# Kernel tuning notes

Measured on AMD Instinct MI355X. Metric: run time of the kernel, lower is better.

## Reference

```python
import jax, jax.numpy as jnp
import numpy as np

B, P, D, E, A, V, T = 128, 49, 512, 512, 512, 10000, 50


def _lstm_cell(x, h, c, w_ih, w_hh, b_ih, b_hh):
    # torch.nn.LSTMCell gate order: i, f, g, o
    g = x @ w_ih.T + b_ih + h @ w_hh.T + b_hh
    i, f, gg, o = jnp.split(g, 4, axis=1)
    c_new = jax.nn.sigmoid(f) * c + jax.nn.sigmoid(i) * jnp.tanh(gg)
    h_new = jax.nn.sigmoid(o) * jnp.tanh(c_new)
    return h_new, c_new


def _forward(spatial_feature, global_image, emb, w_ih1, w_hh1, b_ih1, b_hh1,
             s_wx, s_bx, s_wh, s_bh, w_ih2, w_hh2, b_ih2, b_hh2,
             aff_s_w, aff_s_b, aff_h_w, aff_h_b, ws_w, ws_b, wg_w, wg_b,
             wv_w, wv_b, wh_w, wh_b, wp_w, wp_b, fc_w, fc_b, encoded_captions):
    Bz, Tz = encoded_captions.shape
    embs = jnp.take(emb, encoded_captions, axis=0)                 # (B, T, E)
    gi = jnp.broadcast_to(global_image[:, None, :], (Bz, Tz, global_image.shape[-1]))
    x_word = jnp.concatenate([embs, gi], axis=-1)[:, :-1]          # (B, T-1, 2E) = [w_t; v^g]
    visual_att = spatial_feature @ wv_w.T + wv_b                   # (B, P, A); loop-invariant, hoisted

    def step(carry, x_t):
        h1, m1, h2, m2 = carry
        # ---- LSTM-1 on [h_last^2; w_t; v^g] ----
        x1 = jnp.concatenate([h2, x_t], axis=1)                    # (B, D + 2E)
        h1n, m1n = _lstm_cell(x1, h1, m1, w_ih1, w_hh1, b_ih1, b_hh1)
        # visual sentinel (dropout = identity in eval mode); uses h_{t-1}^1 and m_t^1
        s_t = jax.nn.sigmoid(x1 @ s_wx.T + s_bx + h1 @ s_wh.T + s_bh) * jnp.tanh(m1n)
        # ---- adaptive attention ----
        s2 = jax.nn.relu(s_t @ aff_s_w.T + aff_s_b)
        ht = jnp.tanh(h1n @ aff_h_w.T + aff_h_b)
        hid = ht @ wg_w.T + wg_b                                   # (B, A)
        sen = s2 @ ws_w.T + ws_b                                   # (B, A)
        ext = jnp.tanh(jnp.concatenate([visual_att, sen[:, None, :]], axis=1) + hid[:, None, :])
        z = jnp.squeeze(ext @ wh_w.T + wh_b, axis=2)               # (B, P+1)
        alpha = jax.nn.softmax(z, axis=1)
        concat_feat = jnp.concatenate([spatial_feature, s2[:, None, :]], axis=1)
        c_hat = jnp.sum(concat_feat * alpha[:, :, None], axis=1)   # (B, D)
        att_out = jnp.tanh((c_hat + ht) @ wp_w.T + wp_b)           # c_t
        # ---- LSTM-2 on [c_t; h_t^1] ----
        x2 = jnp.concatenate([att_out, h1n], axis=1)
        h2n, m2n = _lstm_cell(x2, h2, m2, w_ih2, w_hh2, b_ih2, b_hh2)
        preds = h2n @ fc_w.T + fc_b                                # fc(dropout(h2)); dropout = identity
        return (h1n, m1n, h2n, m2n), preds

    z0 = jnp.zeros((Bz, w_hh1.shape[1]), dtype=spatial_feature.dtype)
    _, preds = jax.lax.scan(step, (z0, z0, z0, z0), jnp.swapaxes(x_word, 0, 1))
    return jnp.swapaxes(preds, 0, 1)                               # (B, T-1, V)


def setup_inputs() -> dict:
    key = jax.random.key(0)
    ks = iter(jax.random.split(key, 40))
    def nrm(shape, scale=0.05):
        return jax.random.normal(next(ks), shape, dtype=jnp.float32) * scale
    return dict(
        spatial_feature=nrm((B, P, D), 1.0),
        global_image=nrm((B, E), 1.0),
        encoded_captions=jax.random.randint(next(ks), (B, T), 0, V),
        caption_lengths=jnp.full((B, 1), T, dtype=jnp.int32),  # all full-length => sort/truncation are no-ops
        emb=nrm((V, E)),
        w_ih1=nrm((4 * D, 2 * E + D)), w_hh1=nrm((4 * D, D)), b_ih1=nrm((4 * D,)), b_hh1=nrm((4 * D,)),
        s_wx=nrm((D, 2 * E + D)), s_bx=nrm((D,)), s_wh=nrm((D, D)), s_bh=nrm((D,)),
        w_ih2=nrm((4 * D, 2 * D)), w_hh2=nrm((4 * D, D)), b_ih2=nrm((4 * D,)), b_hh2=nrm((4 * D,)),
        aff_s_w=nrm((D, D)), aff_s_b=nrm((D,)),
        aff_h_w=nrm((D, D)), aff_h_b=nrm((D,)),
        ws_w=nrm((A, D)), ws_b=nrm((A,)),
        wg_w=nrm((A, D)), wg_b=nrm((A,)),
        wv_w=nrm((A, D)), wv_b=nrm((A,)),
        wh_w=nrm((1, A)), wh_b=nrm((1,)),
        wp_w=nrm((D, D)), wp_b=nrm((D,)),
        fc_w=nrm((V, D)), fc_b=nrm((V,)),
    )


def reference(spatial_feature, global_image, encoded_captions, caption_lengths, emb,
              w_ih1, w_hh1, b_ih1, b_hh1, s_wx, s_bx, s_wh, s_bh,
              w_ih2, w_hh2, b_ih2, b_hh2, aff_s_w, aff_s_b, aff_h_w, aff_h_b,
              ws_w, ws_b, wg_w, wg_b, wv_w, wv_b, wh_w, wh_b, wp_w, wp_b, fc_w, fc_b):
    # caption_lengths are all == T here, so decode_lengths == T-1 for every row
    # and the original sort + shrinking-batch logic is an identity.
    del caption_lengths
    return _forward(spatial_feature, global_image, emb, w_ih1, w_hh1, b_ih1, b_hh1,
                    s_wx, s_bx, s_wh, s_bh, w_ih2, w_hh2, b_ih2, b_hh2,
                    aff_s_w, aff_s_b, aff_h_w, aff_h_b, ws_w, ws_b, wg_w, wg_b,
                    wv_w, wv_b, wh_w, wh_b, wp_w, wp_b, fc_w, fc_b, encoded_captions)
```

## Files before the change

kernel.cpp:

```cpp
#include <hip/hip_runtime.h>


typedef unsigned short u16;
typedef short bf16x8 __attribute__((ext_vector_type(8)));
typedef float f32x4 __attribute__((ext_vector_type(4)));

#define MFMA16(a, b, c) __builtin_amdgcn_mfma_f32_16x16x32_bf16(a, b, c, 0, 0, 0)

__device__ __forceinline__ u16 f2bf(float f) {
    union { float f; unsigned u; } v; v.f = f;
    return (u16)((v.u + 0x7fffu + ((v.u >> 16) & 1u)) >> 16);
}
__device__ __forceinline__ float bf2f(u16 h) {
    union { unsigned u; float f; } v; v.u = ((unsigned)h) << 16; return v.f;
}
__device__ __forceinline__ float sigm(float x) {
    x = fminf(fmaxf(x, -30.f), 30.f);
    return 1.f / (1.f + __expf(-x));
}
__device__ __forceinline__ float tanh_(float x) {
    x = fminf(fmaxf(x, -15.f), 15.f);
    float e = __expf(2.f * x);
    return (e - 1.f) / (e + 1.f);
}

__device__ __forceinline__ void gemm_2x4(const u16* __restrict__ A0, const u16* __restrict__ A1,
                                         int asplit, int lda0, int lda1,
                                         const u16* __restrict__ W, int ldw, int K,
                                         int m_base, int n_base, int nt, f32x4 acc[2][4]) {
    const int lane = threadIdx.x & 63, r = lane & 15, lg = lane >> 4;
    for (int k0 = 0; k0 < K; k0 += 32) {
        int kk = k0 + lg * 8;
        const u16* Ab; int ka, lda;
        if (k0 < asplit) { Ab = A0; ka = kk; lda = lda0; }
        else             { Ab = A1; ka = kk - asplit; lda = lda1; }
        bf16x8 a0 = *(const bf16x8*)(Ab + (size_t)(m_base + r) * lda + ka);
        bf16x8 a1 = *(const bf16x8*)(Ab + (size_t)(m_base + 16 + r) * lda + ka);
#pragma unroll
        for (int j = 0; j < 4; ++j) {
            if (j < nt) {
                bf16x8 wf = *(const bf16x8*)(W + (size_t)(n_base + j * 16 + r) * ldw + kk);
                acc[0][j] = MFMA16(a0, wf, acc[0][j]);
                acc[1][j] = MFMA16(a1, wf, acc[1][j]);
            }
        }
    }
}


__global__ __launch_bounds__(256) void k_cvt(const float* __restrict__ s, u16* __restrict__ d, int n) {
    int i = blockIdx.x * 256 + threadIdx.x;
    if (i < n) d[i] = f2bf(s[i]);
}

__global__ __launch_bounds__(256) void k_pack(const float* __restrict__ A, int ldA, int offA, int wA,
                                              const float* __restrict__ Bs, int ldB,
                                              u16* __restrict__ dst, int Ktot, int total) {
    int i = blockIdx.x * 256 + threadIdx.x;
    if (i >= total) return;
    int n = i / Ktot, k = i - n * Ktot;
    float v = (k < wA) ? A[(size_t)n * ldA + offA + k] : Bs[(size_t)n * ldB + (k - wA)];
    dst[i] = f2bf(v);
}

__global__ __launch_bounds__(256) void k_xw(const float* __restrict__ emb, const float* __restrict__ gimg,
                                            const int* __restrict__ cap, u16* __restrict__ XW, int total) {
    int i = blockIdx.x * 256 + threadIdx.x;
    if (i >= total) return;
    int t = i >> 17;
    int rem = i & ((1 << 17) - 1);
    int b = rem >> 10, k = rem & 1023;
    float v = (k < 512) ? emb[(size_t)cap[b * 50 + t] * 512 + k] : gimg[b * 512 + (k - 512)];
    XW[i] = f2bf(v);
}


__global__ __launch_bounds__(256) void k_p1ps(const u16* __restrict__ XW, const u16* __restrict__ W1X,
                                              const u16* __restrict__ WSX,
                                              const float* __restrict__ b_ih1, const float* __restrict__ b_hh1,
                                              const float* __restrict__ s_bx, const float* __restrict__ s_bh,
                                              float* __restrict__ P1, float* __restrict__ PS) {
    int bid = blockIdx.x;
    int ng = bid % 40, mg = bid / 40;
    int w = threadIdx.x >> 6, lane = threadIdx.x & 63, r = lane & 15, lg = lane >> 4;
    int m_base = mg * 128 + w * 32;
    f32x4 acc[2][4] = {};
    if (ng < 32) {
        int n_base = ng * 64;
        gemm_2x4(XW, XW, 1 << 28, 1024, 1024, W1X, 1024, 1024, m_base, n_base, 4, acc);
#pragma unroll
        for (int mt = 0; mt < 2; ++mt)
#pragma unroll
            for (int j = 0; j < 4; ++j)
#pragma unroll
                for (int reg = 0; reg < 4; ++reg) {
                    int row = m_base + mt * 16 + lg * 4 + reg;
                    int col = n_base + j * 16 + r;
                    P1[(size_t)row * 2048 + col] = acc[mt][j][reg] + b_ih1[col] + b_hh1[col];
                }
    } else {
        int n_base = (ng - 32) * 64;
        gemm_2x4(XW, XW, 1 << 28, 1024, 1024, WSX, 1024, 1024, m_base, n_base, 4, acc);
#pragma unroll
        for (int mt = 0; mt < 2; ++mt)
#pragma unroll
            for (int j = 0; j < 4; ++j)
#pragma unroll
                for (int reg = 0; reg < 4; ++reg) {
                    int row = m_base + mt * 16 + lg * 4 + reg;
                    int col = n_base + j * 16 + r;
                    PS[(size_t)row * 512 + col] = acc[mt][j][reg] + s_bx[col] + s_bh[col];
                }
    }
}

__global__ __launch_bounds__(256) void k_va(const u16* __restrict__ SPB, const u16* __restrict__ WVB,
                                            const float* __restrict__ wv_b, float* __restrict__ VA) {
    int bid = blockIdx.x;
    int ng = bid % 8, mg = bid / 8;
    int w = threadIdx.x >> 6, lane = threadIdx.x & 63, r = lane & 15, lg = lane >> 4;
    int m_base = mg * 128 + w * 32;
    int n_base = ng * 64;
    f32x4 acc[2][4] = {};
    gemm_2x4(SPB, SPB, 1 << 28, 512, 512, WVB, 512, 512, m_base, n_base, 4, acc);
#pragma unroll
    for (int mt = 0; mt < 2; ++mt)
#pragma unroll
        for (int j = 0; j < 4; ++j)
#pragma unroll
            for (int reg = 0; reg < 4; ++reg) {
                int row = m_base + mt * 16 + lg * 4 + reg;
                int col = n_base + j * 16 + r;
                VA[(size_t)row * 512 + col] = acc[mt][j][reg] + wv_b[col];
            }
}


__global__ __launch_bounds__(256) void k_lstm1(const u16* __restrict__ H2BF, const u16* __restrict__ H1C,
                                               const u16* __restrict__ W1H, const u16* __restrict__ WSH,
                                               const float* __restrict__ P1, const float* __restrict__ PS,
                                               float* __restrict__ M1, u16* __restrict__ H1N,
                                               u16* __restrict__ STBF, int t) {
    int d0 = blockIdx.x * 16;
    int w = threadIdx.x >> 6, lane = threadIdx.x & 63, r = lane & 15, lg = lane >> 4;
    int m_base = w * 32;
    f32x4 acc[2][5] = {};
    for (int k0 = 0; k0 < 1024; k0 += 32) {
        int kk = k0 + lg * 8;
        const u16* Ab = (k0 < 512) ? H2BF : H1C;
        int ka = (k0 < 512) ? kk : kk - 512;
        bf16x8 a0 = *(const bf16x8*)(Ab + (size_t)(m_base + r) * 512 + ka);
        bf16x8 a1 = *(const bf16x8*)(Ab + (size_t)(m_base + 16 + r) * 512 + ka);
#pragma unroll
        for (int gt = 0; gt < 4; ++gt) {
            bf16x8 wf = *(const bf16x8*)(W1H + (size_t)(gt * 512 + d0 + r) * 1024 + kk);
            acc[0][gt] = MFMA16(a0, wf, acc[0][gt]);
            acc[1][gt] = MFMA16(a1, wf, acc[1][gt]);
        }
        bf16x8 wsf = *(const bf16x8*)(WSH + (size_t)(d0 + r) * 1024 + kk);
        acc[0][4] = MFMA16(a0, wsf, acc[0][4]);
        acc[1][4] = MFMA16(a1, wsf, acc[1][4]);
    }
    int d = d0 + r;
#pragma unroll
    for (int mt = 0; mt < 2; ++mt)
#pragma unroll
        for (int reg = 0; reg < 4; ++reg) {
            int row = m_base + mt * 16 + lg * 4 + reg;
            const float* p1r = P1 + ((size_t)t * 128 + row) * 2048;
            float gi = acc[mt][0][reg] + p1r[d];
            float gf = acc[mt][1][reg] + p1r[512 + d];
            float gg = acc[mt][2][reg] + p1r[1024 + d];
            float go = acc[mt][3][reg] + p1r[1536 + d];
            float gs = acc[mt][4][reg] + PS[((size_t)t * 128 + row) * 512 + d];
            int idx = row * 512 + d;
            float m1o = M1[idx];
            float m1n = sigm(gf) * m1o + sigm(gi) * tanh_(gg);
            float h1n = sigm(go) * tanh_(m1n);
            float st  = sigm(gs) * tanh_(m1n);
            M1[idx] = m1n;
            H1N[idx] = f2bf(h1n);
            STBF[idx] = f2bf(st);
        }
}

__global__ __launch_bounds__(256) void k_ph2(const u16* __restrict__ STBF, const u16* __restrict__ H1N,
                                             const u16* __restrict__ H2BF,
                                             const u16* __restrict__ AFFS, const u16* __restrict__ AFFH,
                                             const u16* __restrict__ W2H,
                                             const float* __restrict__ affs_b, const float* __restrict__ affh_b,
                                             u16* __restrict__ S2BF, float* __restrict__ HTF,
                                             u16* __restrict__ HTBF, float* __restrict__ G2P) {
    int bid = blockIdx.x;
    int w = threadIdx.x >> 6, lane = threadIdx.x & 63, r = lane & 15, lg = lane >> 4;
    int m_base = w * 32;
    f32x4 acc[2][4] = {};
    if (bid < 8) {
        int n_base = bid * 64;
        gemm_2x4(STBF, STBF, 1 << 28, 512, 512, AFFS, 512, 512, m_base, n_base, 4, acc);
#pragma unroll
        for (int mt = 0; mt < 2; ++mt)
#pragma unroll
            for (int j = 0; j < 4; ++j)
#pragma unroll
                for (int reg = 0; reg < 4; ++reg) {
                    int row = m_base + mt * 16 + lg * 4 + reg;
                    int col = n_base + j * 16 + r;
                    float v = acc[mt][j][reg] + affs_b[col];
                    S2BF[row * 512 + col] = f2bf(fmaxf(v, 0.f));
                }
    } else if (bid < 16) {
        int n_base = (bid - 8) * 64;
        gemm_2x4(H1N, H1N, 1 << 28, 512, 512, AFFH, 512, 512, m_base, n_base, 4, acc);
#pragma unroll
        for (int mt = 0; mt < 2; ++mt)
#pragma unroll
            for (int j = 0; j < 4; ++j)
#pragma unroll
                for (int reg = 0; reg < 4; ++reg) {
                    int row = m_base + mt * 16 + lg * 4 + reg;
                    int col = n_base + j * 16 + r;
                    float v = tanh_(acc[mt][j][reg] + affh_b[col]);
                    HTF[row * 512 + col] = v;
                    HTBF[row * 512 + col] = f2bf(v);
                }
    } else {
        int n_base = (bid - 16) * 64;
        gemm_2x4(H1N, H2BF, 512, 512, 512, W2H, 1024, 1024, m_base, n_base, 4, acc);
#pragma unroll
        for (int mt = 0; mt < 2; ++mt)
#pragma unroll
            for (int j = 0; j < 4; ++j)
#pragma unroll
                for (int reg = 0; reg < 4; ++reg) {
                    int row = m_base + mt * 16 + lg * 4 + reg;
                    int col = n_base + j * 16 + r;
                    G2P[row * 2048 + col] = acc[mt][j][reg];
                }
    }
}

__global__ __launch_bounds__(256) void k_ph3(const u16* __restrict__ HTBF, const u16* __restrict__ S2BF,
                                             const u16* __restrict__ WGB, const u16* __restrict__ WSB,
                                             const float* __restrict__ wg_b, const float* __restrict__ ws_b,
                                             float* __restrict__ HID, float* __restrict__ SEN) {
    int bid = blockIdx.x;
    int w = threadIdx.x >> 6, lane = threadIdx.x & 63, r = lane & 15, lg = lane >> 4;
    int m_base = w * 32;
    f32x4 acc[2][4] = {};
    const u16* A = (bid < 8) ? HTBF : S2BF;
    const u16* W = (bid < 8) ? WGB : WSB;
    const float* bb = (bid < 8) ? wg_b : ws_b;
    float* out = (bid < 8) ? HID : SEN;
    int n_base = (bid & 7) * 64;
    gemm_2x4(A, A, 1 << 28, 512, 512, W, 512, 512, m_base, n_base, 4, acc);
#pragma unroll
    for (int mt = 0; mt < 2; ++mt)
#pragma unroll
        for (int j = 0; j < 4; ++j)
#pragma unroll
            for (int reg = 0; reg < 4; ++reg) {
                int row = m_base + mt * 16 + lg * 4 + reg;
                int col = n_base + j * 16 + r;
                out[row * 512 + col] = acc[mt][j][reg] + bb[col];
            }
}

__global__ __launch_bounds__(256) void k_attn(const float* __restrict__ VA, const float* __restrict__ SEN,
                                              const float* __restrict__ HID, const float* __restrict__ whw,
                                              const float* __restrict__ whb, const float* __restrict__ SF,
                                              const u16* __restrict__ S2BF, const float* __restrict__ HTF,
                                              u16* __restrict__ CHHBF) {
    __shared__ float hidL[512], whwL[512], zbuf[50], albuf[50];
    int b = blockIdx.x, tid = threadIdx.x;
    for (int i = tid; i < 512; i += 256) { hidL[i] = HID[b * 512 + i]; whwL[i] = whw[i]; }
    __syncthreads();
    int w = tid >> 6, lane = tid & 63;
    for (int p = w; p < 50; p += 4) {
        const float* src = (p < 49) ? (VA + ((size_t)b * 49 + p) * 512) : (SEN + (size_t)b * 512);
        float part = 0.f;
#pragma unroll
        for (int it = 0; it < 8; ++it) {
            int a = lane + it * 64;
            part += tanh_(src[a] + hidL[a]) * whwL[a];
        }
#pragma unroll
        for (int off2 = 32; off2; off2 >>= 1) part += __shfl_xor(part, off2, 64);
        if (lane == 0) zbuf[p] = part + whb[0];
    }
    __syncthreads();
    if (tid < 64) {
        float v = (tid < 50) ? zbuf[tid] : -1e30f;
        float mx = v;
#pragma unroll
        for (int off2 = 32; off2; off2 >>= 1) mx = fmaxf(mx, __shfl_xor(mx, off2, 64));
        float e = (tid < 50) ? __expf(v - mx) : 0.f;
        float s = e;
#pragma unroll
        for (int off2 = 32; off2; off2 >>= 1) s += __shfl_xor(s, off2, 64);
        if (tid < 50) albuf[tid] = e / s;
    }
    __syncthreads();
    float a49 = albuf[49];
    for (int d = tid; d < 512; d += 256) {
        float acc = a49 * bf2f(S2BF[b * 512 + d]);
        for (int p = 0; p < 49; ++p) acc += albuf[p] * SF[((size_t)b * 49 + p) * 512 + d];
        float chh = acc + HTF[b * 512 + d];
        CHHBF[b * 512 + d] = f2bf(chh);
    }
}

__global__ __launch_bounds__(256) void k_ph4b(const u16* __restrict__ CHHBF, const u16* __restrict__ WPB,
                                              const float* __restrict__ wp_b, u16* __restrict__ ATTBF) {
    int bid = blockIdx.x;
    int w = threadIdx.x >> 6, lane = threadIdx.x & 63, r = lane & 15, lg = lane >> 4;
    int m_base = w * 32;
    int n_base = bid * 64;
    f32x4 acc[2][4] = {};
    gemm_2x4(CHHBF, CHHBF, 1 << 28, 512, 512, WPB, 512, 512, m_base, n_base, 4, acc);
#pragma unroll
    for (int mt = 0; mt < 2; ++mt)
#pragma unroll
        for (int j = 0; j < 4; ++j)
#pragma unroll
            for (int reg = 0; reg < 4; ++reg) {
                int row = m_base + mt * 16 + lg * 4 + reg;
                int col = n_base + j * 16 + r;
                ATTBF[row * 512 + col] = f2bf(tanh_(acc[mt][j][reg] + wp_b[col]));
            }
}

__global__ __launch_bounds__(256) void k_lstm2(const u16* __restrict__ ATTBF, const u16* __restrict__ W2A,
                                               const float* __restrict__ G2P,
                                               const float* __restrict__ b_ih2, const float* __restrict__ b_hh2,
                                               float* __restrict__ M2, u16* __restrict__ H2BF,
                                               u16* __restrict__ H2ALL, int t) {
    int d0 = blockIdx.x * 16;
    int w = threadIdx.x >> 6, lane = threadIdx.x & 63, r = lane & 15, lg = lane >> 4;
    int m_base = w * 32;
    f32x4 acc[2][4] = {};
    for (int k0 = 0; k0 < 512; k0 += 32) {
        int kk = k0 + lg * 8;
        bf16x8 a0 = *(const bf16x8*)(ATTBF + (size_t)(m_base + r) * 512 + kk);
        bf16x8 a1 = *(const bf16x8*)(ATTBF + (size_t)(m_base + 16 + r) * 512 + kk);
#pragma unroll
        for (int gt = 0; gt < 4; ++gt) {
            bf16x8 wf = *(const bf16x8*)(W2A + (size_t)(gt * 512 + d0 + r) * 512 + kk);
            acc[0][gt] = MFMA16(a0, wf, acc[0][gt]);
            acc[1][gt] = MFMA16(a1, wf, acc[1][gt]);
        }
    }
    int d = d0 + r;
#pragma unroll
    for (int mt = 0; mt < 2; ++mt)
#pragma unroll
        for (int reg = 0; reg < 4; ++reg) {
            int row = m_base + mt * 16 + lg * 4 + reg;
            const float* g2r = G2P + (size_t)row * 2048;
            float gi = acc[mt][0][reg] + g2r[d]        + b_ih2[d]        + b_hh2[d];
            float gf = acc[mt][1][reg] + g2r[512 + d]  + b_ih2[512 + d]  + b_hh2[512 + d];
            float gg = acc[mt][2][reg] + g2r[1024 + d] + b_ih2[1024 + d] + b_hh2[1024 + d];
            float go = acc[mt][3][reg] + g2r[1536 + d] + b_ih2[1536 + d] + b_hh2[1536 + d];
            int idx = row * 512 + d;
            float m2n = sigm(gf) * M2[idx] + sigm(gi) * tanh_(gg);
            float h2n = sigm(go) * tanh_(m2n);
            M2[idx] = m2n;
            u16 hb = f2bf(h2n);
            H2BF[idx] = hb;
            H2ALL[((size_t)t * 128 + row) * 512 + d] = hb;
        }
}

__global__ __launch_bounds__(256) void k_fc(const u16* __restrict__ H2ALL, const u16* __restrict__ FCB,
                                            const float* __restrict__ fc_b, float* __restrict__ out) {
    int bid = blockIdx.x;
    int ng = bid % 157, mg = bid / 157;
    int w = threadIdx.x >> 6, lane = threadIdx.x & 63, r = lane & 15, lg = lane >> 4;
    int m_base = mg * 128 + w * 32;
    int n_base = ng * 64;
    int nt = (10000 - n_base) / 16; if (nt > 4) nt = 4;
    f32x4 acc[2][4] = {};
    gemm_2x4(H2ALL, H2ALL, 1 << 28, 512, 512, FCB, 512, 512, m_base, n_base, nt, acc);
#pragma unroll
    for (int mt = 0; mt < 2; ++mt)
#pragma unroll
        for (int j = 0; j < 4; ++j) {
            if (j < nt) {
#pragma unroll
                for (int reg = 0; reg < 4; ++reg) {
                    int row = m_base + mt * 16 + lg * 4 + reg;
                    int col = n_base + j * 16 + r;
                    int t = row >> 7, b = row & 127;
                    out[((size_t)b * 49 + t) * 10000 + col] = acc[mt][j][reg] + fc_b[col];
                }
            }
        }
}


extern "C" void kernel_launch(void* const* d_in, const int* in_sizes, int n_in,
                              void* d_out, int out_size, void* d_ws, size_t ws_size,
                              hipStream_t stream) {
    (void)in_sizes; (void)n_in; (void)out_size; (void)ws_size;

    const float* SF      = (const float*)d_in[0];
    const float* GIMG    = (const float*)d_in[1];
    const int*   CAP     = (const int*)d_in[2];
    const float* EMB     = (const float*)d_in[4];
    const float* w_ih1   = (const float*)d_in[5];
    const float* w_hh1   = (const float*)d_in[6];
    const float* b_ih1   = (const float*)d_in[7];
    const float* b_hh1   = (const float*)d_in[8];
    const float* s_wx    = (const float*)d_in[9];
    const float* s_bx    = (const float*)d_in[10];
    const float* s_wh    = (const float*)d_in[11];
    const float* s_bh    = (const float*)d_in[12];
    const float* w_ih2   = (const float*)d_in[13];
    const float* w_hh2   = (const float*)d_in[14];
    const float* b_ih2   = (const float*)d_in[15];
    const float* b_hh2   = (const float*)d_in[16];
    const float* aff_s_w = (const float*)d_in[17];
    const float* aff_s_b = (const float*)d_in[18];
    const float* aff_h_w = (const float*)d_in[19];
    const float* aff_h_b = (const float*)d_in[20];
    const float* ws_w    = (const float*)d_in[21];
    const float* ws_b    = (const float*)d_in[22];
    const float* wg_w    = (const float*)d_in[23];
    const float* wg_b    = (const float*)d_in[24];
    const float* wv_w    = (const float*)d_in[25];
    const float* wv_b    = (const float*)d_in[26];
    const float* wh_w    = (const float*)d_in[27];
    const float* wh_b    = (const float*)d_in[28];
    const float* wp_w    = (const float*)d_in[29];
    const float* wp_b    = (const float*)d_in[30];
    const float* fc_w    = (const float*)d_in[31];
    const float* fc_b    = (const float*)d_in[32];

    float* out = (float*)d_out;

    float* P1 = out;
    float* PS = out + 12845056;
    float* VA = out + 16056320;

    char* ws = (char*)d_ws;
    size_t off = 0;
    auto alloc = [&](size_t elts, size_t esz) -> void* {
        void* p = ws + off;
        off += (elts * esz + 255) & ~(size_t)255;
        return p;
    };
    u16* W1H   = (u16*)alloc(2048 * 1024, 2);
    u16* WSH   = (u16*)alloc(512 * 1024, 2);
    u16* W1X   = (u16*)alloc(2048 * 1024, 2);
    u16* WSX   = (u16*)alloc(512 * 1024, 2);
    u16* W2A   = (u16*)alloc(2048 * 512, 2);
    u16* W2H   = (u16*)alloc(2048 * 1024, 2);
    u16* AFFS  = (u16*)alloc(262144, 2);
    u16* AFFH  = (u16*)alloc(262144, 2);
    u16* WSB   = (u16*)alloc(262144, 2);
    u16* WGB   = (u16*)alloc(262144, 2);
    u16* WVB   = (u16*)alloc(262144, 2);
    u16* WPB   = (u16*)alloc(262144, 2);
    u16* FCB   = (u16*)alloc(5120000, 2);
    u16* SPB   = (u16*)alloc(3211264, 2);
    u16* XWB   = (u16*)alloc(6422528, 2);
    u16* H2ALL = (u16*)alloc(3211264, 2);
    u16* H1A   = (u16*)alloc(65536, 2);
    u16* H1B   = (u16*)alloc(65536, 2);
    u16* H2BF  = (u16*)alloc(65536, 2);
    u16* STBF  = (u16*)alloc(65536, 2);
    u16* S2BF  = (u16*)alloc(65536, 2);
    u16* HTBF  = (u16*)alloc(65536, 2);
    u16* CHHBF = (u16*)alloc(65536, 2);
    u16* ATTBF = (u16*)alloc(65536, 2);
    float* M1  = (float*)alloc(65536, 4);
    float* M2  = (float*)alloc(65536, 4);
    float* HTF = (float*)alloc(65536, 4);
    float* HID = (float*)alloc(65536, 4);
    float* SEN = (float*)alloc(65536, 4);
    float* G2P = (float*)alloc(262144, 4);

    hipMemsetAsync(H1A, 0, 65536 * 2, stream);
    hipMemsetAsync(H2BF, 0, 65536 * 2, stream);
    hipMemsetAsync(M1, 0, 65536 * 4, stream);
    hipMemsetAsync(M2, 0, 65536 * 4, stream);

    auto gs = [](int n) { return (n + 255) / 256; };

    k_cvt<<<gs(262144), 256, 0, stream>>>(aff_s_w, AFFS, 262144);
    k_cvt<<<gs(262144), 256, 0, stream>>>(aff_h_w, AFFH, 262144);
    k_cvt<<<gs(262144), 256, 0, stream>>>(ws_w, WSB, 262144);
    k_cvt<<<gs(262144), 256, 0, stream>>>(wg_w, WGB, 262144);
    k_cvt<<<gs(262144), 256, 0, stream>>>(wv_w, WVB, 262144);
    k_cvt<<<gs(262144), 256, 0, stream>>>(wp_w, WPB, 262144);
    k_cvt<<<gs(5120000), 256, 0, stream>>>(fc_w, FCB, 5120000);
    k_cvt<<<gs(3211264), 256, 0, stream>>>(SF, SPB, 3211264);

    k_pack<<<gs(2097152), 256, 0, stream>>>(w_ih1, 1536, 0, 512, w_hh1, 512, W1H, 1024, 2097152);
    k_pack<<<gs(524288), 256, 0, stream>>>(s_wx, 1536, 0, 512, s_wh, 512, WSH, 1024, 524288);
    k_pack<<<gs(2097152), 256, 0, stream>>>(w_ih1, 1536, 512, 1024, w_ih1, 1536, W1X, 1024, 2097152);
    k_pack<<<gs(524288), 256, 0, stream>>>(s_wx, 1536, 512, 1024, s_wx, 1536, WSX, 1024, 524288);
    k_pack<<<gs(1048576), 256, 0, stream>>>(w_ih2, 1024, 0, 512, w_ih2, 1024, W2A, 512, 1048576);
    k_pack<<<gs(2097152), 256, 0, stream>>>(w_ih2, 1024, 512, 512, w_hh2, 512, W2H, 1024, 2097152);

    k_xw<<<gs(6422528), 256, 0, stream>>>(EMB, GIMG, CAP, XWB, 6422528);

    k_p1ps<<<49 * 40, 256, 0, stream>>>(XWB, W1X, WSX, b_ih1, b_hh1, s_bx, s_bh, P1, PS);
    k_va<<<49 * 8, 256, 0, stream>>>(SPB, WVB, wv_b, VA);

    for (int t = 0; t < 49; ++t) {
        const u16* h1c = (t & 1) ? H1B : H1A;
        u16* h1n = (t & 1) ? H1A : H1B;
        k_lstm1<<<32, 256, 0, stream>>>(H2BF, h1c, W1H, WSH, P1, PS, M1, h1n, STBF, t);
        k_ph2<<<48, 256, 0, stream>>>(STBF, h1n, H2BF, AFFS, AFFH, W2H, aff_s_b, aff_h_b,
                                      S2BF, HTF, HTBF, G2P);
        k_ph3<<<16, 256, 0, stream>>>(HTBF, S2BF, WGB, WSB, wg_b, ws_b, HID, SEN);
        k_attn<<<128, 256, 0, stream>>>(VA, SEN, HID, wh_w, wh_b, SF, S2BF, HTF, CHHBF);
        k_ph4b<<<8, 256, 0, stream>>>(CHHBF, WPB, wp_b, ATTBF);
        k_lstm2<<<32, 256, 0, stream>>>(ATTBF, W2A, G2P, b_ih2, b_hh2, M2, H2BF, H2ALL, t);
    }

    k_fc<<<49 * 157, 256, 0, stream>>>(H2ALL, FCB, fc_b, out);
}
```

Before: 6.966 ms.

## Fuse per-timestep decoder kernels into one persistent kernel with grid barriers

Replaces the 49×6 per-step kernel launches with a single persistent 64-block kernel. It separates the phases with atomic-counter grid barriers, using a fresh counter for each barrier. The many weight-conversion and packing launches are also merged into two combined kernels. The goal is to remove launch overhead and inter-kernel gaps in the sequential recurrence. In exchange, co-residency of all 64 blocks is required, many blocks sit idle in the narrow phases, and the spin-wait barriers add their own latency.

```diff
diff --git a/kernel.cpp b/kernel.cpp
--- a/kernel.cpp
+++ b/kernel.cpp
@@ -48,19 +48,49 @@
 }
 
 
-__global__ __launch_bounds__(256) void k_cvt(const float* __restrict__ s, u16* __restrict__ d, int n) {
+__global__ __launch_bounds__(256) void k_cvt8(
+    const float* __restrict__ s0, const float* __restrict__ s1, const float* __restrict__ s2,
+    const float* __restrict__ s3, const float* __restrict__ s4, const float* __restrict__ s5,
+    const float* __restrict__ s6, const float* __restrict__ s7,
+    u16* __restrict__ d0, u16* __restrict__ d1, u16* __restrict__ d2, u16* __restrict__ d3,
+    u16* __restrict__ d4, u16* __restrict__ d5, u16* __restrict__ d6, u16* __restrict__ d7) {
     int i = blockIdx.x * 256 + threadIdx.x;
-    if (i < n) d[i] = f2bf(s[i]);
-}
-
-__global__ __launch_bounds__(256) void k_pack(const float* __restrict__ A, int ldA, int offA, int wA,
-                                              const float* __restrict__ Bs, int ldB,
-                                              u16* __restrict__ dst, int Ktot, int total) {
-    int i = blockIdx.x * 256 + threadIdx.x;
-    if (i >= total) return;
+    const int S = 262144;
+    if (i < 6 * S) {
+        int seg = i >> 18, off = i & (S - 1);
+        const float* s = seg == 0 ? s0 : seg == 1 ? s1 : seg == 2 ? s2 : seg == 3 ? s3 : seg == 4 ? s4 : s5;
+        u16* d = seg == 0 ? d0 : seg == 1 ? d1 : seg == 2 ? d2 : seg == 3 ? d3 : seg == 4 ? d4 : d5;
+        d[off] = f2bf(s[off]);
+    } else if (i < 6 * S + 5120000) {
+        int off = i - 6 * S;
+        d6[off] = f2bf(s6[off]);
+    } else {
+        int off = i - 6 * S - 5120000;
+        if (off < 3211264) d7[off] = f2bf(s7[off]);
+    }
+}
+
+__device__ __forceinline__ void packel(const float* __restrict__ A, int ldA, int offA, int wA,
+                                       const float* __restrict__ Bs, int ldB,
+                                       u16* __restrict__ dst, int Ktot, int i) {
     int n = i / Ktot, k = i - n * Ktot;
     float v = (k < wA) ? A[(size_t)n * ldA + offA + k] : Bs[(size_t)n * ldB + (k - wA)];
     dst[i] = f2bf(v);
+}
+
+__global__ __launch_bounds__(256) void k_pack6(
+    const float* __restrict__ w_ih1, const float* __restrict__ w_hh1,
+    const float* __restrict__ s_wx, const float* __restrict__ s_wh,
+    const float* __restrict__ w_ih2, const float* __restrict__ w_hh2,
+    u16* __restrict__ W1H, u16* __restrict__ WSH, u16* __restrict__ W1X,
+    u16* __restrict__ WSX, u16* __restrict__ W2A, u16* __restrict__ W2H) {
+    int i = blockIdx.x * 256 + threadIdx.x;
+    if      (i < 2097152) packel(w_ih1, 1536, 0, 512, w_hh1, 512, W1H, 1024, i);
+    else if (i < 2621440) packel(s_wx, 1536, 0, 512, s_wh, 512, WSH, 1024, i - 2097152);
+    else if (i < 4718592) packel(w_ih1, 1536, 512, 1024, w_ih1, 1536, W1X, 1024, i - 2621440);
+    else if (i < 5242880) packel(s_wx, 1536, 512, 1024, s_wx, 1536, WSX, 1024, i - 4718592);
+    else if (i < 6291456) packel(w_ih2, 1024, 0, 512, w_ih2, 1024, W2A, 512, i - 5242880);
+    else if (i < 8388608) packel(w_ih2, 1024, 512, 512, w_hh2, 512, W2H, 1024, i - 6291456);
 }
 
 __global__ __launch_bounds__(256) void k_xw(const float* __restrict__ emb, const float* __restrict__ gimg,
@@ -136,12 +166,25 @@
 }
 
 
-__global__ __launch_bounds__(256) void k_lstm1(const u16* __restrict__ H2BF, const u16* __restrict__ H1C,
-                                               const u16* __restrict__ W1H, const u16* __restrict__ WSH,
-                                               const float* __restrict__ P1, const float* __restrict__ PS,
-                                               float* __restrict__ M1, u16* __restrict__ H1N,
-                                               u16* __restrict__ STBF, int t) {
-    int d0 = blockIdx.x * 16;
+#define NBLK 64
+
+__device__ __forceinline__ void grid_barrier(int* bar, int idx) {
+    __syncthreads();
+    if (threadIdx.x == 0) {
+        __threadfence();
+        __hip_atomic_fetch_add(&bar[idx], 1, __ATOMIC_RELAXED, __HIP_MEMORY_SCOPE_AGENT);
+        while (__hip_atomic_load(&bar[idx], __ATOMIC_RELAXED, __HIP_MEMORY_SCOPE_AGENT) < NBLK)
+            __builtin_amdgcn_s_sleep(1);
+        __threadfence();
+    }
+    __syncthreads();
+}
+
+__device__ __forceinline__ void lstm1_body(int bid, const u16* __restrict__ H2BF, const u16* H1C,
+                                           const u16* __restrict__ W1H, const u16* __restrict__ WSH,
+                                           const float* __restrict__ P1, const float* __restrict__ PS,
+                                           float* __restrict__ M1, u16* H1N, u16* __restrict__ STBF, int t) {
+    int d0 = bid * 16;
     int w = threadIdx.x >> 6, lane = threadIdx.x & 63, r = lane & 15, lg = lane >> 4;
     int m_base = w * 32;
     f32x4 acc[2][5] = {};
@@ -184,14 +227,13 @@
         }
 }
 
-__global__ __launch_bounds__(256) void k_ph2(const u16* __restrict__ STBF, const u16* __restrict__ H1N,
-                                             const u16* __restrict__ H2BF,
-                                             const u16* __restrict__ AFFS, const u16* __restrict__ AFFH,
-                                             const u16* __restrict__ W2H,
-                                             const float* __restrict__ affs_b, const float* __restrict__ affh_b,
-                                             u16* __restrict__ S2BF, float* __restrict__ HTF,
-                                             u16* __restrict__ HTBF, float* __restrict__ G2P) {
-    int bid = blockIdx.x;
+__device__ __forceinline__ void ph2_body(int bid, const u16* __restrict__ STBF, const u16* H1N,
+                                         const u16* __restrict__ H2BF,
+                                         const u16* __restrict__ AFFS, const u16* __restrict__ AFFH,
+                                         const u16* __restrict__ W2H,
+                                         const float* __restrict__ affs_b, const float* __restrict__ affh_b,
+                                         u16* __restrict__ S2BF, float* __restrict__ HTF,
+                                         u16* __restrict__ HTBF, float* __restrict__ G2P) {
     int w = threadIdx.x >> 6, lane = threadIdx.x & 63, r = lane & 15, lg = lane >> 4;
     int m_base = w * 32;
     f32x4 acc[2][4] = {};
@@ -240,11 +282,10 @@
     }
 }
 
-__global__ __launch_bounds__(256) void k_ph3(const u16* __restrict__ HTBF, const u16* __restrict__ S2BF,
-                                             const u16* __restrict__ WGB, const u16* __restrict__ WSB,
-                                             const float* __restrict__ wg_b, const float* __restrict__ ws_b,
-                                             float* __restrict__ HID, float* __restrict__ SEN) {
-    int bid = blockIdx.x;
+__device__ __forceinline__ void ph3_body(int bid, const u16* __restrict__ HTBF, const u16* __restrict__ S2BF,
+                                         const u16* __restrict__ WGB, const u16* __restrict__ WSB,
+                                         const float* __restrict__ wg_b, const float* __restrict__ ws_b,
+                                         float* __restrict__ HID, float* __restrict__ SEN) {
     int w = threadIdx.x >> 6, lane = threadIdx.x & 63, r = lane & 15, lg = lane >> 4;
     int m_base = w * 32;
     f32x4 acc[2][4] = {};
@@ -266,13 +307,13 @@
             }
 }
 
-__global__ __launch_bounds__(256) void k_attn(const float* __restrict__ VA, const float* __restrict__ SEN,
-                                              const float* __restrict__ HID, const float* __restrict__ whw,
-                                              const float* __restrict__ whb, const float* __restrict__ SF,
-                                              const u16* __restrict__ S2BF, const float* __restrict__ HTF,
-                                              u16* __restrict__ CHHBF) {
-    __shared__ float hidL[512], whwL[512], zbuf[50], albuf[50];
-    int b = blockIdx.x, tid = threadIdx.x;
+__device__ __forceinline__ void attn_body(int b, const float* __restrict__ VA, const float* __restrict__ SEN,
+                                          const float* __restrict__ HID, const float* __restrict__ whw,
+                                          const float* __restrict__ whb, const float* __restrict__ SF,
+                                          const u16* __restrict__ S2BF, const float* __restrict__ HTF,
+                                          u16* __restrict__ CHHBF,
+                                          float* hidL, float* whwL, float* zbuf, float* albuf) {
+    int tid = threadIdx.x;
     for (int i = tid; i < 512; i += 256) { hidL[i] = HID[b * 512 + i]; whwL[i] = whw[i]; }
     __syncthreads();
     int w = tid >> 6, lane = tid & 63;
@@ -308,11 +349,11 @@
         float chh = acc + HTF[b * 512 + d];
         CHHBF[b * 512 + d] = f2bf(chh);
     }
-}
-
-__global__ __launch_bounds__(256) void k_ph4b(const u16* __restrict__ CHHBF, const u16* __restrict__ WPB,
-                                              const float* __restrict__ wp_b, u16* __restrict__ ATTBF) {
-    int bid = blockIdx.x;
+    __syncthreads();
+}
+
+__device__ __forceinline__ void ph4b_body(int bid, const u16* __restrict__ CHHBF, const u16* __restrict__ WPB,
+                                          const float* __restrict__ wp_b, u16* __restrict__ ATTBF) {
     int w = threadIdx.x >> 6, lane = threadIdx.x & 63, r = lane & 15, lg = lane >> 4;
     int m_base = w * 32;
     int n_base = bid * 64;
@@ -330,12 +371,12 @@
             }
 }
 
-__global__ __launch_bounds__(256) void k_lstm2(const u16* __restrict__ ATTBF, const u16* __restrict__ W2A,
-                                               const float* __restrict__ G2P,
-                                               const float* __restrict__ b_ih2, const float* __restrict__ b_hh2,
-                                               float* __restrict__ M2, u16* __restrict__ H2BF,
-                                               u16* __restrict__ H2ALL, int t) {
-    int d0 = blockIdx.x * 16;
+__device__ __forceinline__ void lstm2_body(int bid, const u16* __restrict__ ATTBF, const u16* __restrict__ W2A,
+                                           const float* __restrict__ G2P,
+                                           const float* __restrict__ b_ih2, const float* __restrict__ b_hh2,
+                                           float* __restrict__ M2, u16* __restrict__ H2BF,
+                                           u16* __restrict__ H2ALL, int t) {
+    int d0 = bid * 16;
     int w = threadIdx.x >> 6, lane = threadIdx.x & 63, r = lane & 15, lg = lane >> 4;
     int m_base = w * 32;
     f32x4 acc[2][4] = {};
@@ -369,6 +410,40 @@
             H2BF[idx] = hb;
             H2ALL[((size_t)t * 128 + row) * 512 + d] = hb;
         }
+}
+
+__global__ __launch_bounds__(256) void k_scan(
+    const u16* __restrict__ W1H, const u16* __restrict__ WSH, const u16* __restrict__ W2A,
+    const u16* __restrict__ W2H, const u16* __restrict__ AFFS, const u16* __restrict__ AFFH,
+    const u16* __restrict__ WSB, const u16* __restrict__ WGB, const u16* __restrict__ WPB,
+    const float* __restrict__ P1, const float* __restrict__ PS, const float* __restrict__ VA,
+    const float* __restrict__ b_ih2, const float* __restrict__ b_hh2,
+    const float* __restrict__ affs_b, const float* __restrict__ affh_b,
+    const float* __restrict__ wg_b, const float* __restrict__ ws_b, const float* __restrict__ wp_b,
+    const float* __restrict__ whw, const float* __restrict__ whb, const float* __restrict__ SF,
+    u16* H1A, u16* H1B, u16* H2BF, u16* STBF, u16* S2BF, u16* HTBF, u16* CHHBF, u16* ATTBF,
+    float* M1, float* M2, float* HTF, float* HID, float* SEN, float* G2P,
+    u16* H2ALL, int* bar) {
+    __shared__ float hidL[512], whwL[512], zbuf[50], albuf[50];
+    int bid = blockIdx.x;
+    int bi = 0;
+    for (int t = 0; t < 49; ++t) {
+        const u16* h1c = (t & 1) ? H1B : H1A;
+        u16* h1n = (t & 1) ? H1A : H1B;
+        if (bid < 32) lstm1_body(bid, H2BF, h1c, W1H, WSH, P1, PS, M1, h1n, STBF, t);
+        grid_barrier(bar, bi++);
+        if (bid < 48) ph2_body(bid, STBF, h1n, H2BF, AFFS, AFFH, W2H, affs_b, affh_b, S2BF, HTF, HTBF, G2P);
+        grid_barrier(bar, bi++);
+        if (bid < 16) ph3_body(bid, HTBF, S2BF, WGB, WSB, wg_b, ws_b, HID, SEN);
+        grid_barrier(bar, bi++);
+        attn_body(bid, VA, SEN, HID, whw, whb, SF, S2BF, HTF, CHHBF, hidL, whwL, zbuf, albuf);
+        attn_body(bid + 64, VA, SEN, HID, whw, whb, SF, S2BF, HTF, CHHBF, hidL, whwL, zbuf, albuf);
+        grid_barrier(bar, bi++);
+        if (bid < 8) ph4b_body(bid, CHHBF, WPB, wp_b, ATTBF);
+        grid_barrier(bar, bi++);
+        if (bid < 32) lstm2_body(bid, ATTBF, W2A, G2P, b_ih2, b_hh2, M2, H2BF, H2ALL, t);
+        grid_barrier(bar, bi++);
+    }
 }
 
 __global__ __launch_bounds__(256) void k_fc(const u16* __restrict__ H2ALL, const u16* __restrict__ FCB,
@@ -479,46 +554,28 @@
     float* HID = (float*)alloc(65536, 4);
     float* SEN = (float*)alloc(65536, 4);
     float* G2P = (float*)alloc(262144, 4);
+    int*   BAR = (int*)alloc(2048, 4);
 
     hipMemsetAsync(H1A, 0, 65536 * 2, stream);
     hipMemsetAsync(H2BF, 0, 65536 * 2, stream);
     hipMemsetAsync(M1, 0, 65536 * 4, stream);
     hipMemsetAsync(M2, 0, 65536 * 4, stream);
-
-    auto gs = [](int n) { return (n + 255) / 256; };
-
-    k_cvt<<<gs(262144), 256, 0, stream>>>(aff_s_w, AFFS, 262144);
-    k_cvt<<<gs(262144), 256, 0, stream>>>(aff_h_w, AFFH, 262144);
-    k_cvt<<<gs(262144), 256, 0, stream>>>(ws_w, WSB, 262144);
-    k_cvt<<<gs(262144), 256, 0, stream>>>(wg_w, WGB, 262144);
-    k_cvt<<<gs(262144), 256, 0, stream>>>(wv_w, WVB, 262144);
-    k_cvt<<<gs(262144), 256, 0, stream>>>(wp_w, WPB, 262144);
-    k_cvt<<<gs(5120000), 256, 0, stream>>>(fc_w, FCB, 5120000);
-    k_cvt<<<gs(3211264), 256, 0, stream>>>(SF, SPB, 3211264);
-
-    k_pack<<<gs(2097152), 256, 0, stream>>>(w_ih1, 1536, 0, 512, w_hh1, 512, W1H, 1024, 2097152);
-    k_pack<<<gs(524288), 256, 0, stream>>>(s_wx, 1536, 0, 512, s_wh, 512, WSH, 1024, 524288);
-    k_pack<<<gs(2097152), 256, 0, stream>>>(w_ih1, 1536, 512, 1024, w_ih1, 1536, W1X, 1024, 2097152);
-    k_pack<<<gs(524288), 256, 0, stream>>>(s_wx, 1536, 512, 1024, s_wx, 1536, WSX, 1024, 524288);
-    k_pack<<<gs(1048576), 256, 0, stream>>>(w_ih2, 1024, 0, 512, w_ih2, 1024, W2A, 512, 1048576);
-    k_pack<<<gs(2097152), 256, 0, stream>>>(w_ih2, 1024, 512, 512, w_hh2, 512, W2H, 1024, 2097152);
-
-    k_xw<<<gs(6422528), 256, 0, stream>>>(EMB, GIMG, CAP, XWB, 6422528);
+    hipMemsetAsync(BAR, 0, 2048 * 4, stream);
+
+    k_cvt8<<<38688, 256, 0, stream>>>(aff_s_w, aff_h_w, ws_w, wg_w, wv_w, wp_w, fc_w, SF,
+                                      AFFS, AFFH, WSB, WGB, WVB, WPB, FCB, SPB);
+    k_pack6<<<32768, 256, 0, stream>>>(w_ih1, w_hh1, s_wx, s_wh, w_ih2, w_hh2,
+                                       W1H, WSH, W1X, WSX, W2A, W2H);
+    k_xw<<<(6422528 + 255) / 256, 256, 0, stream>>>(EMB, GIMG, CAP, XWB, 6422528);
 
     k_p1ps<<<49 * 40, 256, 0, stream>>>(XWB, W1X, WSX, b_ih1, b_hh1, s_bx, s_bh, P1, PS);
     k_va<<<49 * 8, 256, 0, stream>>>(SPB, WVB, wv_b, VA);
 
-    for (int t = 0; t < 49; ++t) {
-        const u16* h1c = (t & 1) ? H1B : H1A;
-        u16* h1n = (t & 1) ? H1A : H1B;
-        k_lstm1<<<32, 256, 0, stream>>>(H2BF, h1c, W1H, WSH, P1, PS, M1, h1n, STBF, t);
-        k_ph2<<<48, 256, 0, stream>>>(STBF, h1n, H2BF, AFFS, AFFH, W2H, aff_s_b, aff_h_b,
-                                      S2BF, HTF, HTBF, G2P);
-        k_ph3<<<16, 256, 0, stream>>>(HTBF, S2BF, WGB, WSB, wg_b, ws_b, HID, SEN);
-        k_attn<<<128, 256, 0, stream>>>(VA, SEN, HID, wh_w, wh_b, SF, S2BF, HTF, CHHBF);
-        k_ph4b<<<8, 256, 0, stream>>>(CHHBF, WPB, wp_b, ATTBF);
-        k_lstm2<<<32, 256, 0, stream>>>(ATTBF, W2A, G2P, b_ih2, b_hh2, M2, H2BF, H2ALL, t);
-    }
+    k_scan<<<NBLK, 256, 0, stream>>>(W1H, WSH, W2A, W2H, AFFS, AFFH, WSB, WGB, WPB,
+                                     P1, PS, VA, b_ih2, b_hh2, aff_s_b, aff_h_b,
+                                     wg_b, ws_b, wp_b, wh_w, wh_b, SF,
+                                     H1A, H1B, H2BF, STBF, S2BF, HTBF, CHHBF, ATTBF,
+                                     M1, M2, HTF, HID, SEN, G2P, H2ALL, BAR);
 
     k_fc<<<49 * 157, 256, 0, stream>>>(H2ALL, FCB, fc_b, out);
 }
```

New measurement: 14.11 ms. 2.03x slower.
